# Kernel optimization log

Measured on AMD Instinct MI355X. Metric: run time of the kernel, lower is better.

Reference implementation:

```python
import jax, jax.numpy as jnp
import numpy as np

D_MODEL = 256
SCALE = jnp.sqrt(jnp.float32(D_MODEL))


def setup_inputs() -> dict:
    key = jax.random.key(0)
    kq, kk, kv = jax.random.split(key, 3)
    B, S, D = 4, 4096, D_MODEL
    Q = jax.random.normal(kq, (B, S, D), dtype=jnp.float32)
    K = jax.random.normal(kk, (B, S, D), dtype=jnp.float32)
    V = jax.random.normal(kv, (B, S, D), dtype=jnp.float32)
    return {"Q": Q, "K": K, "V": V}


def reference(Q, K, V):
    # scores: (B, S, S) = Q @ K^T / sqrt(d_model)
    scores = jnp.einsum('bqd,bkd->bqk', Q, K) / SCALE
    attn = jax.nn.softmax(scores, axis=-1)
    # output: (B, S, D)
    return jnp.einsum('bqk,bkd->bqd', attn, V)
```

## Files before the change

kernel.cpp:

```cpp
#include <hip/hip_runtime.h>
#include <hip/hip_bf16.h>
#include <stdint.h>

#define S_LEN 4096
#define D_DIM 256
#define NBATCH 4
#define NKT 64
#define NSUP 32

typedef unsigned short u16;
typedef float  f32x4  __attribute__((ext_vector_type(4)));
typedef __bf16 bf16x8 __attribute__((ext_vector_type(8)));
typedef __bf16 bf16x4 __attribute__((ext_vector_type(4)));
typedef short  s16x8  __attribute__((ext_vector_type(8)));
typedef short  s16x4  __attribute__((ext_vector_type(4)));

__device__ __forceinline__ f32x4 mfma16(bf16x8 a, bf16x8 b, f32x4 c) {
  return __builtin_amdgcn_mfma_f32_16x16x32_bf16(a, b, c, 0, 0, 0);
}

__device__ __forceinline__ s16x4 cvt4(float x, float y, float z, float w) {
  bf16x4 b;
  b[0] = (__bf16)x; b[1] = (__bf16)y; b[2] = (__bf16)z; b[3] = (__bf16)w;
  return __builtin_bit_cast(s16x4, b);
}

__global__ void convert_bf16_kernel(const float* __restrict__ in,
                                    u16* __restrict__ out, int n4) {
  int i = blockIdx.x * blockDim.x + threadIdx.x;
  if (i >= n4) return;
  float4 f = reinterpret_cast<const float4*>(in)[i];
  reinterpret_cast<s16x4*>(out)[i] = cvt4(f.x, f.y, f.z, f.w);
}


__device__ __forceinline__
void compute_tile(const char* KsB, const char* vpA, const char* vpB,
                  const bf16x8 (&qf)[8], f32x4 (&acc)[16],
                  float& m_run, float& l_run, int g, int h)
{
  const f32x4 fz = {0.f, 0.f, 0.f, 0.f};

  f32x4 st[4];
  __builtin_amdgcn_s_setprio(1);
  #pragma unroll
  for (int t = 0; t < 4; ++t) {
    f32x4 a = fz;
    const int row = t * 16 + h;
    const int sw  = (row & 7) << 4;
    #pragma unroll
    for (int dc = 0; dc < 8; ++dc) {
      s16x8 kfrag = *reinterpret_cast<const s16x8*>(KsB + row * 512 + ((dc * 64 + g * 16) ^ sw));
      a = mfma16(__builtin_bit_cast(bf16x8, kfrag), qf[dc], a);
    }
    st[t] = a;
  }
  __builtin_amdgcn_s_setprio(0);

  float sv[16];
  #pragma unroll
  for (int t = 0; t < 4; ++t) {
    sv[t * 4 + 0] = st[t][0]; sv[t * 4 + 1] = st[t][1];
    sv[t * 4 + 2] = st[t][2]; sv[t * 4 + 3] = st[t][3];
  }
  float tmax = sv[0];
  #pragma unroll
  for (int i = 1; i < 16; ++i) tmax = fmaxf(tmax, sv[i]);
  tmax = fmaxf(tmax, __shfl_xor(tmax, 16));
  tmax = fmaxf(tmax, __shfl_xor(tmax, 32));

  if (!__all(tmax <= m_run + 8.0f)) {
    const float mnew  = fmaxf(m_run, tmax);
    const float alpha = __expf(m_run - mnew);
    l_run *= alpha;
    const float af0 = __shfl(alpha, g * 4 + 0);
    const float af1 = __shfl(alpha, g * 4 + 1);
    const float af2 = __shfl(alpha, g * 4 + 2);
    const float af3 = __shfl(alpha, g * 4 + 3);
    #pragma unroll
    for (int dt = 0; dt < 16; ++dt) {
      acc[dt][0] *= af0; acc[dt][1] *= af1; acc[dt][2] *= af2; acc[dt][3] *= af3;
    }
    m_run = mnew;
  }

  float psum = 0.f;
  #pragma unroll
  for (int i = 0; i < 16; ++i) { sv[i] = __expf(sv[i] - m_run); psum += sv[i]; }
  psum += __shfl_xor(psum, 16);
  psum += __shfl_xor(psum, 32);
  l_run += psum;

  bf16x8 pa0, pa1;
  #pragma unroll
  for (int j = 0; j < 8; ++j) { pa0[j] = (__bf16)sv[j]; pa1[j] = (__bf16)sv[8 + j]; }

  __builtin_amdgcn_s_setprio(1);
  #pragma unroll
  for (int dt = 0; dt < 16; ++dt) {
    s16x8 v0 = *reinterpret_cast<const s16x8*>(vpA + dt * 2048);
    s16x8 v1 = *reinterpret_cast<const s16x8*>(vpB + dt * 2048);
    acc[dt] = mfma16(pa0, __builtin_bit_cast(bf16x8, v0), acc[dt]);
    acc[dt] = mfma16(pa1, __builtin_bit_cast(bf16x8, v1), acc[dt]);
  }
  __builtin_amdgcn_s_setprio(0);
}

template<bool USE_WS>
__global__ __launch_bounds__(512, 1)
void attn_fwd_kernel(const float* __restrict__ Qg, const void* __restrict__ Kp,
                     const void* __restrict__ Vp, float* __restrict__ Og)
{
  __shared__ __align__(16) char smem[131072];

  const int wg   = blockIdx.x;
  const int swz  = (wg & 7) * 32 + (wg >> 3);
  const int b    = swz >> 6;
  const int qt   = swz & 63;
  const int tid  = threadIdx.x;
  const int wave = tid >> 6;
  const int lane = tid & 63;
  const int g    = lane >> 4;
  const int h    = lane & 15;
  const int gid  = tid >> 8;
  const int ltid = tid & 255;
  const int wq   = wave & 3;

  const int kb  = ltid & 15;
  const int dcq = ltid >> 4;

  char* KsB = smem + gid * 65536;
  char* VtB = KsB + 32768;

  const int qbase = qt * 64 + wq * 16;

  bf16x8 qf[8];
  {
    const float* qrow = Qg + ((size_t)b * S_LEN + qbase + h) * D_DIM;
    #pragma unroll
    for (int dc = 0; dc < 8; ++dc) {
      float4 f0 = *reinterpret_cast<const float4*>(qrow + dc * 32 + g * 8);
      float4 f1 = *reinterpret_cast<const float4*>(qrow + dc * 32 + g * 8 + 4);
      bf16x8 q;
      q[0] = (__bf16)(f0.x * 0.0625f); q[1] = (__bf16)(f0.y * 0.0625f);
      q[2] = (__bf16)(f0.z * 0.0625f); q[3] = (__bf16)(f0.w * 0.0625f);
      q[4] = (__bf16)(f1.x * 0.0625f); q[5] = (__bf16)(f1.y * 0.0625f);
      q[6] = (__bf16)(f1.z * 0.0625f); q[7] = (__bf16)(f1.w * 0.0625f);
      qf[dc] = q;
    }
  }

  f32x4 acc[16];
  const f32x4 fz = {0.f, 0.f, 0.f, 0.f};
  #pragma unroll
  for (int i = 0; i < 16; ++i) acc[i] = fz;
  float m_run = -1e30f;
  float l_run = 0.f;

  const char* vpA = VtB + h * 128 + ((32 * g)      ^ ((h & 7) << 4));
  const char* vpB = VtB + h * 128 + ((32 * g + 16) ^ ((h & 7) << 4));

  if constexpr (USE_WS) {
    const u16* Kb = (const u16*)Kp + (size_t)b * S_LEN * D_DIM;
    const u16* Vb = (const u16*)Vp + (size_t)b * S_LEN * D_DIM;

    const u16* ksrc = Kb + (size_t)(ltid >> 5) * D_DIM + (ltid & 31) * 8;
    char*      kdst = KsB + (ltid >> 5) * 512 + (((ltid & 31) * 16) ^ ((ltid >> 5) << 4));
    const u16* vsrc = Vb + (size_t)(kb * 4) * D_DIM + dcq * 16;
    const int  Xw   = 32 * (kb & 3) + 8 * (kb >> 2);

    s16x8 kreg[8], vlo[4], vhi[4];

    {
      const size_t nb = (size_t)gid * 64 * D_DIM;
      #pragma unroll
      for (int i = 0; i < 8; ++i)
        kreg[i] = *reinterpret_cast<const s16x8*>(ksrc + nb + (size_t)i * 8 * D_DIM);
      #pragma unroll
      for (int r = 0; r < 4; ++r) {
        const u16* s = vsrc + nb + (size_t)r * D_DIM;
        vlo[r] = *reinterpret_cast<const s16x8*>(s);
        vhi[r] = *reinterpret_cast<const s16x8*>(s + 8);
      }
      #pragma unroll
      for (int i = 0; i < 8; ++i)
        *reinterpret_cast<s16x8*>(kdst + i * 4096) = kreg[i];
      #pragma unroll
      for (int j = 0; j < 8; ++j) {
        s16x4 c0, c1;
        c0[0] = vlo[0][j]; c0[1] = vlo[1][j]; c0[2] = vlo[2][j]; c0[3] = vlo[3][j];
        c1[0] = vhi[0][j]; c1[1] = vhi[1][j]; c1[2] = vhi[2][j]; c1[3] = vhi[3][j];
        const int d0 = dcq * 16 + j;
        const int d1 = d0 + 8;
        *reinterpret_cast<s16x4*>(VtB + d0 * 128 + (Xw ^ ((d0 & 7) << 4))) = c0;
        *reinterpret_cast<s16x4*>(VtB + d1 * 128 + (Xw ^ ((d1 & 7) << 4))) = c1;
      }
    }
    __syncthreads();

    for (int s = 0; s < NSUP - 1; ++s) {
      const size_t nb = (size_t)(2 * (s + 1) + gid) * 64 * D_DIM;
      #pragma unroll
      for (int i = 0; i < 8; ++i)
        kreg[i] = *reinterpret_cast<const s16x8*>(ksrc + nb + (size_t)i * 8 * D_DIM);
      #pragma unroll
      for (int r = 0; r < 4; ++r) {
        const u16* sp = vsrc + nb + (size_t)r * D_DIM;
        vlo[r] = *reinterpret_cast<const s16x8*>(sp);
        vhi[r] = *reinterpret_cast<const s16x8*>(sp + 8);
      }

      compute_tile(KsB, vpA, vpB, qf, acc, m_run, l_run, g, h);

      __syncthreads();
      #pragma unroll
      for (int i = 0; i < 8; ++i)
        *reinterpret_cast<s16x8*>(kdst + i * 4096) = kreg[i];
      #pragma unroll
      for (int j = 0; j < 8; ++j) {
        s16x4 c0, c1;
        c0[0] = vlo[0][j]; c0[1] = vlo[1][j]; c0[2] = vlo[2][j]; c0[3] = vlo[3][j];
        c1[0] = vhi[0][j]; c1[1] = vhi[1][j]; c1[2] = vhi[2][j]; c1[3] = vhi[3][j];
        const int d0 = dcq * 16 + j;
        const int d1 = d0 + 8;
        *reinterpret_cast<s16x4*>(VtB + d0 * 128 + (Xw ^ ((d0 & 7) << 4))) = c0;
        *reinterpret_cast<s16x4*>(VtB + d1 * 128 + (Xw ^ ((d1 & 7) << 4))) = c1;
      }
      __syncthreads();
    }
    compute_tile(KsB, vpA, vpB, qf, acc, m_run, l_run, g, h);

  } else {
    const float* Kf = (const float*)Kp + (size_t)b * S_LEN * D_DIM;
    const float* Vf = (const float*)Vp + (size_t)b * S_LEN * D_DIM;
    for (int s = 0; s < NSUP; ++s) {
      const int kt = 2 * s + gid;
      __syncthreads();
      #pragma unroll
      for (int i = 0; i < 16; ++i) {
        int flat = i * 256 + ltid;
        int kk = flat >> 6;
        int d  = (flat & 63) * 4;
        float4 fk = *reinterpret_cast<const float4*>(Kf + (size_t)(kt * 64 + kk) * D_DIM + d);
        *reinterpret_cast<s16x4*>(KsB + kk * 512 + ((d * 2) ^ ((kk & 7) << 4))) = cvt4(fk.x, fk.y, fk.z, fk.w);
      }
      {
        s16x8 lo[4], hi[4];
        #pragma unroll
        for (int r = 0; r < 4; ++r) {
          const float* src = Vf + (size_t)(kt * 64 + kb * 4 + r) * D_DIM + dcq * 16;
          float4 f0 = *reinterpret_cast<const float4*>(src);
          float4 f1 = *reinterpret_cast<const float4*>(src + 4);
          float4 f2 = *reinterpret_cast<const float4*>(src + 8);
          float4 f3 = *reinterpret_cast<const float4*>(src + 12);
          lo[r] = __builtin_shufflevector(cvt4(f0.x, f0.y, f0.z, f0.w),
                                          cvt4(f1.x, f1.y, f1.z, f1.w), 0, 1, 2, 3, 4, 5, 6, 7);
          hi[r] = __builtin_shufflevector(cvt4(f2.x, f2.y, f2.z, f2.w),
                                          cvt4(f3.x, f3.y, f3.z, f3.w), 0, 1, 2, 3, 4, 5, 6, 7);
        }
        const int Xw = 32 * (kb & 3) + 8 * (kb >> 2);
        #pragma unroll
        for (int j = 0; j < 8; ++j) {
          s16x4 c0, c1;
          c0[0] = lo[0][j]; c0[1] = lo[1][j]; c0[2] = lo[2][j]; c0[3] = lo[3][j];
          c1[0] = hi[0][j]; c1[1] = hi[1][j]; c1[2] = hi[2][j]; c1[3] = hi[3][j];
          const int d0 = dcq * 16 + j;
          const int d1 = d0 + 8;
          *reinterpret_cast<s16x4*>(VtB + d0 * 128 + (Xw ^ ((d0 & 7) << 4))) = c0;
          *reinterpret_cast<s16x4*>(VtB + d1 * 128 + (Xw ^ ((d1 & 7) << 4))) = c1;
        }
      }
      __syncthreads();
      compute_tile(KsB, vpA, vpB, qf, acc, m_run, l_run, g, h);
    }
  }

  __syncthreads();
  float2* mlM = reinterpret_cast<float2*>(smem + 65536);
  if (gid == 1) {
    const int bw = wave - 4;
    char* base = smem + bw * 16384 + lane * 256;
    #pragma unroll
    for (int dt = 0; dt < 16; ++dt) {
      float4 v; v.x = acc[dt][0]; v.y = acc[dt][1]; v.z = acc[dt][2]; v.w = acc[dt][3];
      *reinterpret_cast<float4*>(base + (dt * 16 ^ ((lane & 7) << 4))) = v;
    }
    if (g == 0) { float2 ml; ml.x = m_run; ml.y = l_run; mlM[bw * 16 + h] = ml; }
  }
  __syncthreads();
  if (gid == 0) {
    const float2 ml = mlM[wave * 16 + h];
    const float mB = ml.x, lB = ml.y;
    const float m  = fmaxf(m_run, mB);
    const float sA = __expf(m_run - m);
    const float sB = __expf(mB - m);
    const float l  = l_run * sA + lB * sB;
    float aA[4], aB[4], inv[4];
    #pragma unroll
    for (int r = 0; r < 4; ++r) {
      aA[r]  = __shfl(sA, g * 4 + r);
      aB[r]  = __shfl(sB, g * 4 + r);
      inv[r] = 1.f / __shfl(l, g * 4 + r);
    }
    const char* base = smem + wave * 16384 + lane * 256;
    float* orow0 = Og + ((size_t)b * S_LEN + qbase) * D_DIM;
    #pragma unroll
    for (int dt = 0; dt < 16; ++dt) {
      float4 ab = *reinterpret_cast<const float4*>(base + (dt * 16 ^ ((lane & 7) << 4)));
      orow0[(size_t)(g * 4 + 0) * D_DIM + h + dt * 16] = (acc[dt][0] * aA[0] + ab.x * aB[0]) * inv[0];
      orow0[(size_t)(g * 4 + 1) * D_DIM + h + dt * 16] = (acc[dt][1] * aA[1] + ab.y * aB[1]) * inv[1];
      orow0[(size_t)(g * 4 + 2) * D_DIM + h + dt * 16] = (acc[dt][2] * aA[2] + ab.z * aB[2]) * inv[2];
      orow0[(size_t)(g * 4 + 3) * D_DIM + h + dt * 16] = (acc[dt][3] * aA[3] + ab.w * aB[3]) * inv[3];
    }
  }
}

extern "C" void kernel_launch(void* const* d_in, const int* in_sizes, int n_in,
                              void* d_out, int out_size, void* d_ws, size_t ws_size,
                              hipStream_t stream)
{
  const float* Q = (const float*)d_in[0];
  const float* K = (const float*)d_in[1];
  const float* V = (const float*)d_in[2];
  float* O = (float*)d_out;

  const size_t nelem = (size_t)NBATCH * S_LEN * D_DIM;
  const size_t need  = 2 * nelem * sizeof(u16);

  if (ws_size >= need) {
    u16* Kb = (u16*)d_ws;
    u16* Vb = Kb + nelem;
    int n4 = (int)(nelem / 4);
    convert_bf16_kernel<<<n4 / 256, 256, 0, stream>>>(K, Kb, n4);
    convert_bf16_kernel<<<n4 / 256, 256, 0, stream>>>(V, Vb, n4);
    attn_fwd_kernel<true><<<256, 512, 0, stream>>>(Q, (const void*)Kb, (const void*)Vb, O);
  } else {
    attn_fwd_kernel<false><<<256, 512, 0, stream>>>(Q, (const void*)K, (const void*)V, O);
  }
}
```

Measured before the change: 152.8 us.

## Split KV across four wave groups with 32-row tiles and two query subtiles per wave

Each wave now processes two 16-row query subtiles, so every K and V fragment read from LDS feeds two MFMAs. The KV range is split into four interleaved streams of 32-row tiles instead of two streams of 64-row tiles, and the partial results are combined in a two-stage tree at the end. K tiles are now copied straight from global memory into LDS with global_load_lds instead of passing through registers. The aim is to cut LDS read traffic and register staging, but it doubles accumulator registers and adds merge synchronisation. It also declares launch_bounds(512,2) while using about 130 KB of LDS, which is likely to leave one block per CU anyway.

```diff
diff --git a/kernel.cpp b/kernel.cpp
--- a/kernel.cpp
+++ b/kernel.cpp
@@ -5,7 +5,8 @@
 #define S_LEN 4096
 #define D_DIM 256
 #define NBATCH 4
-#define NKT 64
+#define KVBLK 32
+#define NT 128
 #define NSUP 32
 
 typedef unsigned short u16;
@@ -15,6 +16,9 @@
 typedef short  s16x8  __attribute__((ext_vector_type(8)));
 typedef short  s16x4  __attribute__((ext_vector_type(4)));
 
+#define AS1 __attribute__((address_space(1)))
+#define AS3 __attribute__((address_space(3)))
+
 __device__ __forceinline__ f32x4 mfma16(bf16x8 a, bf16x8 b, f32x4 c) {
   return __builtin_amdgcn_mfma_f32_16x16x32_bf16(a, b, c, 0, 0, 0);
 }
@@ -23,6 +27,11 @@
   bf16x4 b;
   b[0] = (__bf16)x; b[1] = (__bf16)y; b[2] = (__bf16)z; b[3] = (__bf16)w;
   return __builtin_bit_cast(s16x4, b);
+}
+
+__device__ __forceinline__ void gload16(const void* g, void* l) {
+  __builtin_amdgcn_global_load_lds((const AS1 unsigned int*)g,
+                                   (AS3 unsigned int*)l, 16, 0, 0);
 }
 
 __global__ void convert_bf16_kernel(const float* __restrict__ in,
@@ -35,83 +44,86 @@
 
 
 __device__ __forceinline__
-void compute_tile(const char* KsB, const char* vpA, const char* vpB,
-                  const bf16x8 (&qf)[8], f32x4 (&acc)[16],
-                  float& m_run, float& l_run, int g, int h)
+void compute_tile2(const char* KsB, const char* VtB,
+                   const bf16x8 (&qf)[2][8], f32x4 (&acc)[2][16],
+                   float (&m_run)[2], float (&l_run)[2], int g, int h)
 {
   const f32x4 fz = {0.f, 0.f, 0.f, 0.f};
 
-  f32x4 st[4];
+  f32x4 st[2][2];
+  st[0][0] = fz; st[0][1] = fz; st[1][0] = fz; st[1][1] = fz;
   __builtin_amdgcn_s_setprio(1);
   #pragma unroll
-  for (int t = 0; t < 4; ++t) {
-    f32x4 a = fz;
+  for (int t = 0; t < 2; ++t) {
     const int row = t * 16 + h;
     const int sw  = (row & 7) << 4;
     #pragma unroll
     for (int dc = 0; dc < 8; ++dc) {
-      s16x8 kfrag = *reinterpret_cast<const s16x8*>(KsB + row * 512 + ((dc * 64 + g * 16) ^ sw));
-      a = mfma16(__builtin_bit_cast(bf16x8, kfrag), qf[dc], a);
-    }
-    st[t] = a;
+      s16x8 kf = *reinterpret_cast<const s16x8*>(KsB + row * 512 + ((dc * 64 + g * 16) ^ sw));
+      st[0][t] = mfma16(__builtin_bit_cast(bf16x8, kf), qf[0][dc], st[0][t]);
+      st[1][t] = mfma16(__builtin_bit_cast(bf16x8, kf), qf[1][dc], st[1][t]);
+    }
   }
   __builtin_amdgcn_s_setprio(0);
 
-  float sv[16];
+  bf16x8 pa[2];
   #pragma unroll
-  for (int t = 0; t < 4; ++t) {
-    sv[t * 4 + 0] = st[t][0]; sv[t * 4 + 1] = st[t][1];
-    sv[t * 4 + 2] = st[t][2]; sv[t * 4 + 3] = st[t][3];
-  }
-  float tmax = sv[0];
-  #pragma unroll
-  for (int i = 1; i < 16; ++i) tmax = fmaxf(tmax, sv[i]);
-  tmax = fmaxf(tmax, __shfl_xor(tmax, 16));
-  tmax = fmaxf(tmax, __shfl_xor(tmax, 32));
-
-  if (!__all(tmax <= m_run + 8.0f)) {
-    const float mnew  = fmaxf(m_run, tmax);
-    const float alpha = __expf(m_run - mnew);
-    l_run *= alpha;
-    const float af0 = __shfl(alpha, g * 4 + 0);
-    const float af1 = __shfl(alpha, g * 4 + 1);
-    const float af2 = __shfl(alpha, g * 4 + 2);
-    const float af3 = __shfl(alpha, g * 4 + 3);
-    #pragma unroll
-    for (int dt = 0; dt < 16; ++dt) {
-      acc[dt][0] *= af0; acc[dt][1] *= af1; acc[dt][2] *= af2; acc[dt][3] *= af3;
-    }
-    m_run = mnew;
-  }
-
-  float psum = 0.f;
-  #pragma unroll
-  for (int i = 0; i < 16; ++i) { sv[i] = __expf(sv[i] - m_run); psum += sv[i]; }
-  psum += __shfl_xor(psum, 16);
-  psum += __shfl_xor(psum, 32);
-  l_run += psum;
-
-  bf16x8 pa0, pa1;
-  #pragma unroll
-  for (int j = 0; j < 8; ++j) { pa0[j] = (__bf16)sv[j]; pa1[j] = (__bf16)sv[8 + j]; }
+  for (int qs = 0; qs < 2; ++qs) {
+    float sv[8];
+    #pragma unroll
+    for (int t = 0; t < 2; ++t) {
+      sv[t * 4 + 0] = st[qs][t][0]; sv[t * 4 + 1] = st[qs][t][1];
+      sv[t * 4 + 2] = st[qs][t][2]; sv[t * 4 + 3] = st[qs][t][3];
+    }
+    float tmax = sv[0];
+    #pragma unroll
+    for (int i = 1; i < 8; ++i) tmax = fmaxf(tmax, sv[i]);
+    tmax = fmaxf(tmax, __shfl_xor(tmax, 16));
+    tmax = fmaxf(tmax, __shfl_xor(tmax, 32));
+
+    if (!__all(tmax <= m_run[qs] + 8.0f)) {
+      const float mnew  = fmaxf(m_run[qs], tmax);
+      const float alpha = __expf(m_run[qs] - mnew);
+      l_run[qs] *= alpha;
+      float af[4];
+      #pragma unroll
+      for (int r = 0; r < 4; ++r) af[r] = __shfl(alpha, g * 4 + r);
+      #pragma unroll
+      for (int dt = 0; dt < 16; ++dt) {
+        acc[qs][dt][0] *= af[0]; acc[qs][dt][1] *= af[1];
+        acc[qs][dt][2] *= af[2]; acc[qs][dt][3] *= af[3];
+      }
+      m_run[qs] = mnew;
+    }
+
+    float psum = 0.f;
+    #pragma unroll
+    for (int i = 0; i < 8; ++i) { sv[i] = __expf(sv[i] - m_run[qs]); psum += sv[i]; }
+    psum += __shfl_xor(psum, 16);
+    psum += __shfl_xor(psum, 32);
+    l_run[qs] += psum;
+
+    #pragma unroll
+    for (int j = 0; j < 8; ++j) pa[qs][j] = (__bf16)sv[j];
+  }
 
   __builtin_amdgcn_s_setprio(1);
   #pragma unroll
   for (int dt = 0; dt < 16; ++dt) {
-    s16x8 v0 = *reinterpret_cast<const s16x8*>(vpA + dt * 2048);
-    s16x8 v1 = *reinterpret_cast<const s16x8*>(vpB + dt * 2048);
-    acc[dt] = mfma16(pa0, __builtin_bit_cast(bf16x8, v0), acc[dt]);
-    acc[dt] = mfma16(pa1, __builtin_bit_cast(bf16x8, v1), acc[dt]);
+    const int d = dt * 16 + h;
+    s16x8 vf = *reinterpret_cast<const s16x8*>(VtB + d * 64 + ((16 * g) ^ (((dt ^ h) & 3) << 4)));
+    acc[0][dt] = mfma16(pa[0], __builtin_bit_cast(bf16x8, vf), acc[0][dt]);
+    acc[1][dt] = mfma16(pa[1], __builtin_bit_cast(bf16x8, vf), acc[1][dt]);
   }
   __builtin_amdgcn_s_setprio(0);
 }
 
 template<bool USE_WS>
-__global__ __launch_bounds__(512, 1)
+__global__ __launch_bounds__(512, 2)
 void attn_fwd_kernel(const float* __restrict__ Qg, const void* __restrict__ Kp,
                      const void* __restrict__ Vp, float* __restrict__ Og)
 {
-  __shared__ __align__(16) char smem[131072];
+  __shared__ __align__(16) char smem[133120];
 
   const int wg   = blockIdx.x;
   const int swz  = (wg & 7) * 32 + (wg >> 3);
@@ -122,21 +134,24 @@
   const int lane = tid & 63;
   const int g    = lane >> 4;
   const int h    = lane & 15;
-  const int gid  = tid >> 8;
-  const int ltid = tid & 255;
-  const int wq   = wave & 3;
-
-  const int kb  = ltid & 15;
-  const int dcq = ltid >> 4;
-
-  char* KsB = smem + gid * 65536;
-  char* VtB = KsB + 32768;
-
-  const int qbase = qt * 64 + wq * 16;
-
-  bf16x8 qf[8];
-  {
-    const float* qrow = Qg + ((size_t)b * S_LEN + qbase + h) * D_DIM;
+  const int gid  = wave >> 1;
+  const int wq   = wave & 1;
+  const int ltid = tid & 127;
+
+  const int kb  = ltid & 7;
+  const int dcq = ltid >> 3;
+  const int Xw  = 16 * (kb & 3) + 8 * (kb >> 2);
+
+  char* KsB = smem + gid * 32768;
+  char* VtB = KsB + 16384;
+  float2* mlS = reinterpret_cast<float2*>(smem + 131072);
+
+  const int qbase = qt * 64 + wq * 32;
+
+  bf16x8 qf[2][8];
+  #pragma unroll
+  for (int qs = 0; qs < 2; ++qs) {
+    const float* qrow = Qg + ((size_t)b * S_LEN + qbase + qs * 16 + h) * D_DIM;
     #pragma unroll
     for (int dc = 0; dc < 8; ++dc) {
       float4 f0 = *reinterpret_cast<const float4*>(qrow + dc * 32 + g * 8);
@@ -146,45 +161,45 @@
       q[2] = (__bf16)(f0.z * 0.0625f); q[3] = (__bf16)(f0.w * 0.0625f);
       q[4] = (__bf16)(f1.x * 0.0625f); q[5] = (__bf16)(f1.y * 0.0625f);
       q[6] = (__bf16)(f1.z * 0.0625f); q[7] = (__bf16)(f1.w * 0.0625f);
-      qf[dc] = q;
-    }
-  }
-
-  f32x4 acc[16];
+      qf[qs][dc] = q;
+    }
+  }
+
+  f32x4 acc[2][16];
   const f32x4 fz = {0.f, 0.f, 0.f, 0.f};
   #pragma unroll
-  for (int i = 0; i < 16; ++i) acc[i] = fz;
-  float m_run = -1e30f;
-  float l_run = 0.f;
-
-  const char* vpA = VtB + h * 128 + ((32 * g)      ^ ((h & 7) << 4));
-  const char* vpB = VtB + h * 128 + ((32 * g + 16) ^ ((h & 7) << 4));
+  for (int qs = 0; qs < 2; ++qs)
+    #pragma unroll
+    for (int i = 0; i < 16; ++i) acc[qs][i] = fz;
+  float m_run[2] = {-1e30f, -1e30f};
+  float l_run[2] = {0.f, 0.f};
 
   if constexpr (USE_WS) {
     const u16* Kb = (const u16*)Kp + (size_t)b * S_LEN * D_DIM;
     const u16* Vb = (const u16*)Vp + (size_t)b * S_LEN * D_DIM;
 
-    const u16* ksrc = Kb + (size_t)(ltid >> 5) * D_DIM + (ltid & 31) * 8;
-    char*      kdst = KsB + (ltid >> 5) * 512 + (((ltid & 31) * 16) ^ ((ltid >> 5) << 4));
+    const int kb0     = wq * 16 + (lane >> 5);
+    const int colbase = (lane & 31) * 8;
+
     const u16* vsrc = Vb + (size_t)(kb * 4) * D_DIM + dcq * 16;
-    const int  Xw   = 32 * (kb & 3) + 8 * (kb >> 2);
-
-    s16x8 kreg[8], vlo[4], vhi[4];
+
+    s16x8 vlo[4], vhi[4];
 
     {
-      const size_t nb = (size_t)gid * 64 * D_DIM;
-      #pragma unroll
-      for (int i = 0; i < 8; ++i)
-        kreg[i] = *reinterpret_cast<const s16x8*>(ksrc + nb + (size_t)i * 8 * D_DIM);
+      const u16* kt_ptr = Kb + (size_t)gid * KVBLK * D_DIM;
+      #pragma unroll
+      for (int i = 0; i < 8; ++i) {
+        const int k = kb0 + 2 * i;
+        gload16(kt_ptr + k * 256 + (colbase ^ ((k & 7) << 3)),
+                KsB + wq * 8192 + i * 1024);
+      }
+      const size_t nb = (size_t)gid * KVBLK * D_DIM;
       #pragma unroll
       for (int r = 0; r < 4; ++r) {
         const u16* s = vsrc + nb + (size_t)r * D_DIM;
         vlo[r] = *reinterpret_cast<const s16x8*>(s);
         vhi[r] = *reinterpret_cast<const s16x8*>(s + 8);
       }
-      #pragma unroll
-      for (int i = 0; i < 8; ++i)
-        *reinterpret_cast<s16x8*>(kdst + i * 4096) = kreg[i];
       #pragma unroll
       for (int j = 0; j < 8; ++j) {
         s16x4 c0, c1;
@@ -192,17 +207,14 @@
         c1[0] = vhi[0][j]; c1[1] = vhi[1][j]; c1[2] = vhi[2][j]; c1[3] = vhi[3][j];
         const int d0 = dcq * 16 + j;
         const int d1 = d0 + 8;
-        *reinterpret_cast<s16x4*>(VtB + d0 * 128 + (Xw ^ ((d0 & 7) << 4))) = c0;
-        *reinterpret_cast<s16x4*>(VtB + d1 * 128 + (Xw ^ ((d1 & 7) << 4))) = c1;
+        *reinterpret_cast<s16x4*>(VtB + d0 * 64 + (Xw ^ ((((d0 >> 4) ^ d0) & 3) << 4))) = c0;
+        *reinterpret_cast<s16x4*>(VtB + d1 * 64 + (Xw ^ ((((d1 >> 4) ^ d1) & 3) << 4))) = c1;
       }
     }
     __syncthreads();
 
     for (int s = 0; s < NSUP - 1; ++s) {
-      const size_t nb = (size_t)(2 * (s + 1) + gid) * 64 * D_DIM;
-      #pragma unroll
-      for (int i = 0; i < 8; ++i)
-        kreg[i] = *reinterpret_cast<const s16x8*>(ksrc + nb + (size_t)i * 8 * D_DIM);
+      const size_t nb = (size_t)(4 * (s + 1) + gid) * KVBLK * D_DIM;
       #pragma unroll
       for (int r = 0; r < 4; ++r) {
         const u16* sp = vsrc + nb + (size_t)r * D_DIM;
@@ -210,12 +222,18 @@
         vhi[r] = *reinterpret_cast<const s16x8*>(sp + 8);
       }
 
-      compute_tile(KsB, vpA, vpB, qf, acc, m_run, l_run, g, h);
+      compute_tile2(KsB, VtB, qf, acc, m_run, l_run, g, h);
 
       __syncthreads();
-      #pragma unroll
-      for (int i = 0; i < 8; ++i)
-        *reinterpret_cast<s16x8*>(kdst + i * 4096) = kreg[i];
+      {
+        const u16* kt_ptr = Kb + nb;
+        #pragma unroll
+        for (int i = 0; i < 8; ++i) {
+          const int k = kb0 + 2 * i;
+          gload16(kt_ptr + k * 256 + (colbase ^ ((k & 7) << 3)),
+                  KsB + wq * 8192 + i * 1024);
+        }
+      }
       #pragma unroll
       for (int j = 0; j < 8; ++j) {
         s16x4 c0, c1;
@@ -223,32 +241,34 @@
         c1[0] = vhi[0][j]; c1[1] = vhi[1][j]; c1[2] = vhi[2][j]; c1[3] = vhi[3][j];
         const int d0 = dcq * 16 + j;
         const int d1 = d0 + 8;
-        *reinterpret_cast<s16x4*>(VtB + d0 * 128 + (Xw ^ ((d0 & 7) << 4))) = c0;
-        *reinterpret_cast<s16x4*>(VtB + d1 * 128 + (Xw ^ ((d1 & 7) << 4))) = c1;
+        *reinterpret_cast<s16x4*>(VtB + d0 * 64 + (Xw ^ ((((d0 >> 4) ^ d0) & 3) << 4))) = c0;
+        *reinterpret_cast<s16x4*>(VtB + d1 * 64 + (Xw ^ ((((d1 >> 4) ^ d1) & 3) << 4))) = c1;
       }
       __syncthreads();
     }
-    compute_tile(KsB, vpA, vpB, qf, acc, m_run, l_run, g, h);
+    compute_tile2(KsB, VtB, qf, acc, m_run, l_run, g, h);
 
   } else {
     const float* Kf = (const float*)Kp + (size_t)b * S_LEN * D_DIM;
     const float* Vf = (const float*)Vp + (size_t)b * S_LEN * D_DIM;
+    const int rk = ltid >> 2, ck = ltid & 3;
     for (int s = 0; s < NSUP; ++s) {
-      const int kt = 2 * s + gid;
+      const int tile = 4 * s + gid;
       __syncthreads();
       #pragma unroll
-      for (int i = 0; i < 16; ++i) {
-        int flat = i * 256 + ltid;
-        int kk = flat >> 6;
-        int d  = (flat & 63) * 4;
-        float4 fk = *reinterpret_cast<const float4*>(Kf + (size_t)(kt * 64 + kk) * D_DIM + d);
-        *reinterpret_cast<s16x4*>(KsB + kk * 512 + ((d * 2) ^ ((kk & 7) << 4))) = cvt4(fk.x, fk.y, fk.z, fk.w);
+      for (int i = 0; i < 8; ++i) {
+        const float* src = Kf + (size_t)(tile * KVBLK + rk) * D_DIM + ck * 64 + i * 8;
+        float4 f0 = *reinterpret_cast<const float4*>(src);
+        float4 f1 = *reinterpret_cast<const float4*>(src + 4);
+        char* dst = KsB + rk * 512 + ((ck * 128 + i * 16) ^ ((rk & 7) << 4));
+        *reinterpret_cast<s16x4*>(dst)     = cvt4(f0.x, f0.y, f0.z, f0.w);
+        *reinterpret_cast<s16x4*>(dst + 8) = cvt4(f1.x, f1.y, f1.z, f1.w);
       }
       {
         s16x8 lo[4], hi[4];
         #pragma unroll
         for (int r = 0; r < 4; ++r) {
-          const float* src = Vf + (size_t)(kt * 64 + kb * 4 + r) * D_DIM + dcq * 16;
+          const float* src = Vf + (size_t)(tile * KVBLK + kb * 4 + r) * D_DIM + dcq * 16;
           float4 f0 = *reinterpret_cast<const float4*>(src);
           float4 f1 = *reinterpret_cast<const float4*>(src + 4);
           float4 f2 = *reinterpret_cast<const float4*>(src + 8);
@@ -258,7 +278,6 @@
           hi[r] = __builtin_shufflevector(cvt4(f2.x, f2.y, f2.z, f2.w),
                                           cvt4(f3.x, f3.y, f3.z, f3.w), 0, 1, 2, 3, 4, 5, 6, 7);
         }
-        const int Xw = 32 * (kb & 3) + 8 * (kb >> 2);
         #pragma unroll
         for (int j = 0; j < 8; ++j) {
           s16x4 c0, c1;
@@ -266,51 +285,94 @@
           c1[0] = hi[0][j]; c1[1] = hi[1][j]; c1[2] = hi[2][j]; c1[3] = hi[3][j];
           const int d0 = dcq * 16 + j;
           const int d1 = d0 + 8;
-          *reinterpret_cast<s16x4*>(VtB + d0 * 128 + (Xw ^ ((d0 & 7) << 4))) = c0;
-          *reinterpret_cast<s16x4*>(VtB + d1 * 128 + (Xw ^ ((d1 & 7) << 4))) = c1;
+          *reinterpret_cast<s16x4*>(VtB + d0 * 64 + (Xw ^ ((((d0 >> 4) ^ d0) & 3) << 4))) = c0;
+          *reinterpret_cast<s16x4*>(VtB + d1 * 64 + (Xw ^ ((((d1 >> 4) ^ d1) & 3) << 4))) = c1;
         }
       }
       __syncthreads();
-      compute_tile(KsB, vpA, vpB, qf, acc, m_run, l_run, g, h);
+      compute_tile2(KsB, VtB, qf, acc, m_run, l_run, g, h);
     }
   }
 
   __syncthreads();
-  float2* mlM = reinterpret_cast<float2*>(smem + 65536);
+  if (gid >= 2) {
+    char* base = smem + ((gid - 2) * 2 + wq) * 32768 + lane * 512;
+    #pragma unroll
+    for (int qs = 0; qs < 2; ++qs)
+      #pragma unroll
+      for (int dt = 0; dt < 16; ++dt)
+        *reinterpret_cast<f32x4*>(base + (((qs * 16 + dt) * 16) ^ ((lane & 7) << 4))) = acc[qs][dt];
+    if (lane < 16) {
+      float2 a; a.x = m_run[0]; a.y = l_run[0]; mlS[wave * 32 + lane]      = a;
+      float2 c; c.x = m_run[1]; c.y = l_run[1]; mlS[wave * 32 + 16 + lane] = c;
+    }
+  }
+  __syncthreads();
+  if (gid < 2) {
+    const int pw = (gid + 2) * 2 + wq;
+    const char* base = smem + (gid * 2 + wq) * 32768 + lane * 512;
+    #pragma unroll
+    for (int qs = 0; qs < 2; ++qs) {
+      const float2 mlB = mlS[pw * 32 + qs * 16 + h];
+      const float mN = fmaxf(m_run[qs], mlB.x);
+      const float sA = __expf(m_run[qs] - mN);
+      const float sB = __expf(mlB.x - mN);
+      l_run[qs] = l_run[qs] * sA + mlB.y * sB;
+      m_run[qs] = mN;
+      float aA[4], aB[4];
+      #pragma unroll
+      for (int r = 0; r < 4; ++r) { aA[r] = __shfl(sA, g * 4 + r); aB[r] = __shfl(sB, g * 4 + r); }
+      #pragma unroll
+      for (int dt = 0; dt < 16; ++dt) {
+        f32x4 ab = *reinterpret_cast<const f32x4*>(base + (((qs * 16 + dt) * 16) ^ ((lane & 7) << 4)));
+        acc[qs][dt][0] = acc[qs][dt][0] * aA[0] + ab[0] * aB[0];
+        acc[qs][dt][1] = acc[qs][dt][1] * aA[1] + ab[1] * aB[1];
+        acc[qs][dt][2] = acc[qs][dt][2] * aA[2] + ab[2] * aB[2];
+        acc[qs][dt][3] = acc[qs][dt][3] * aA[3] + ab[3] * aB[3];
+      }
+    }
+  }
+  __syncthreads();
   if (gid == 1) {
-    const int bw = wave - 4;
-    char* base = smem + bw * 16384 + lane * 256;
-    #pragma unroll
-    for (int dt = 0; dt < 16; ++dt) {
-      float4 v; v.x = acc[dt][0]; v.y = acc[dt][1]; v.z = acc[dt][2]; v.w = acc[dt][3];
-      *reinterpret_cast<float4*>(base + (dt * 16 ^ ((lane & 7) << 4))) = v;
-    }
-    if (g == 0) { float2 ml; ml.x = m_run; ml.y = l_run; mlM[bw * 16 + h] = ml; }
+    char* base = smem + wq * 32768 + lane * 512;
+    #pragma unroll
+    for (int qs = 0; qs < 2; ++qs)
+      #pragma unroll
+      for (int dt = 0; dt < 16; ++dt)
+        *reinterpret_cast<f32x4*>(base + (((qs * 16 + dt) * 16) ^ ((lane & 7) << 4))) = acc[qs][dt];
+    if (lane < 16) {
+      float2 a; a.x = m_run[0]; a.y = l_run[0]; mlS[wave * 32 + lane]      = a;
+      float2 c; c.x = m_run[1]; c.y = l_run[1]; mlS[wave * 32 + 16 + lane] = c;
+    }
   }
   __syncthreads();
   if (gid == 0) {
-    const float2 ml = mlM[wave * 16 + h];
-    const float mB = ml.x, lB = ml.y;
-    const float m  = fmaxf(m_run, mB);
-    const float sA = __expf(m_run - m);
-    const float sB = __expf(mB - m);
-    const float l  = l_run * sA + lB * sB;
-    float aA[4], aB[4], inv[4];
-    #pragma unroll
-    for (int r = 0; r < 4; ++r) {
-      aA[r]  = __shfl(sA, g * 4 + r);
-      aB[r]  = __shfl(sB, g * 4 + r);
-      inv[r] = 1.f / __shfl(l, g * 4 + r);
-    }
-    const char* base = smem + wave * 16384 + lane * 256;
+    const int pw = 2 + wq;
+    const char* base = smem + wq * 32768 + lane * 512;
     float* orow0 = Og + ((size_t)b * S_LEN + qbase) * D_DIM;
     #pragma unroll
-    for (int dt = 0; dt < 16; ++dt) {
-      float4 ab = *reinterpret_cast<const float4*>(base + (dt * 16 ^ ((lane & 7) << 4)));
-      orow0[(size_t)(g * 4 + 0) * D_DIM + h + dt * 16] = (acc[dt][0] * aA[0] + ab.x * aB[0]) * inv[0];
-      orow0[(size_t)(g * 4 + 1) * D_DIM + h + dt * 16] = (acc[dt][1] * aA[1] + ab.y * aB[1]) * inv[1];
-      orow0[(size_t)(g * 4 + 2) * D_DIM + h + dt * 16] = (acc[dt][2] * aA[2] + ab.z * aB[2]) * inv[2];
-      orow0[(size_t)(g * 4 + 3) * D_DIM + h + dt * 16] = (acc[dt][3] * aA[3] + ab.w * aB[3]) * inv[3];
+    for (int qs = 0; qs < 2; ++qs) {
+      const float2 mlB = mlS[pw * 32 + qs * 16 + h];
+      const float mN = fmaxf(m_run[qs], mlB.x);
+      const float sA = __expf(m_run[qs] - mN);
+      const float sB = __expf(mlB.x - mN);
+      const float lN = l_run[qs] * sA + mlB.y * sB;
+      float aA[4], aB[4], inv[4];
+      #pragma unroll
+      for (int r = 0; r < 4; ++r) {
+        aA[r]  = __shfl(sA, g * 4 + r);
+        aB[r]  = __shfl(sB, g * 4 + r);
+        inv[r] = 1.f / __shfl(lN, g * 4 + r);
+      }
+      #pragma unroll
+      for (int dt = 0; dt < 16; ++dt) {
+        f32x4 ab = *reinterpret_cast<const f32x4*>(base + (((qs * 16 + dt) * 16) ^ ((lane & 7) << 4)));
+        #pragma unroll
+        for (int r = 0; r < 4; ++r) {
+          orow0[(size_t)(qs * 16 + g * 4 + r) * D_DIM + dt * 16 + h] =
+              (acc[qs][dt][r] * aA[r] + ab[r] * aB[r]) * inv[r];
+        }
+      }
     }
   }
 }
```

New measurement: 273.1 us. 78.7% more time.

## Ping-pong compute and tile staging between the two thread groups

Applied to the files above, without the earlier changes.

Replaces register-prefetch double buffering with a schedule where the two 256-thread groups alternate: one group computes on its smem tile while the other stages the next K/V tile into its own buffer. This removes the live prefetch registers and aims to hide global-load latency behind compute. In exchange, only half the waves issue MFMA at any given time, which may serialize the matrix work.

```diff
diff --git a/kernel.cpp b/kernel.cpp
--- a/kernel.cpp
+++ b/kernel.cpp
@@ -104,6 +104,36 @@
     acc[dt] = mfma16(pa1, __builtin_bit_cast(bf16x8, v1), acc[dt]);
   }
   __builtin_amdgcn_s_setprio(0);
+}
+
+__device__ __forceinline__
+void stage_tile(int T, const u16* ksrc, char* kdst,
+                const u16* vsrc, char* VtB, int Xw, int dcq)
+{
+  const size_t nb = (size_t)T * 64 * D_DIM;
+  s16x8 kreg[8], vlo[4], vhi[4];
+  #pragma unroll
+  for (int i = 0; i < 8; ++i)
+    kreg[i] = *reinterpret_cast<const s16x8*>(ksrc + nb + (size_t)i * 8 * D_DIM);
+  #pragma unroll
+  for (int r = 0; r < 4; ++r) {
+    const u16* s = vsrc + nb + (size_t)r * D_DIM;
+    vlo[r] = *reinterpret_cast<const s16x8*>(s);
+    vhi[r] = *reinterpret_cast<const s16x8*>(s + 8);
+  }
+  #pragma unroll
+  for (int i = 0; i < 8; ++i)
+    *reinterpret_cast<s16x8*>(kdst + i * 4096) = kreg[i];
+  #pragma unroll
+  for (int j = 0; j < 8; ++j) {
+    s16x4 c0, c1;
+    c0[0] = vlo[0][j]; c0[1] = vlo[1][j]; c0[2] = vlo[2][j]; c0[3] = vlo[3][j];
+    c1[0] = vhi[0][j]; c1[1] = vhi[1][j]; c1[2] = vhi[2][j]; c1[3] = vhi[3][j];
+    const int d0 = dcq * 16 + j;
+    const int d1 = d0 + 8;
+    *reinterpret_cast<s16x4*>(VtB + d0 * 128 + (Xw ^ ((d0 & 7) << 4))) = c0;
+    *reinterpret_cast<s16x4*>(VtB + d1 * 128 + (Xw ^ ((d1 & 7) << 4))) = c1;
+  }
 }
 
 template<bool USE_WS>
@@ -128,6 +158,7 @@
 
   const int kb  = ltid & 15;
   const int dcq = ltid >> 4;
+  const int Xw  = 32 * (kb & 3) + 8 * (kb >> 2);
 
   char* KsB = smem + gid * 65536;
   char* VtB = KsB + 32768;
@@ -167,68 +198,18 @@
     const u16* ksrc = Kb + (size_t)(ltid >> 5) * D_DIM + (ltid & 31) * 8;
     char*      kdst = KsB + (ltid >> 5) * 512 + (((ltid & 31) * 16) ^ ((ltid >> 5) << 4));
     const u16* vsrc = Vb + (size_t)(kb * 4) * D_DIM + dcq * 16;
-    const int  Xw   = 32 * (kb & 3) + 8 * (kb >> 2);
-
-    s16x8 kreg[8], vlo[4], vhi[4];
-
-    {
-      const size_t nb = (size_t)gid * 64 * D_DIM;
-      #pragma unroll
-      for (int i = 0; i < 8; ++i)
-        kreg[i] = *reinterpret_cast<const s16x8*>(ksrc + nb + (size_t)i * 8 * D_DIM);
-      #pragma unroll
-      for (int r = 0; r < 4; ++r) {
-        const u16* s = vsrc + nb + (size_t)r * D_DIM;
-        vlo[r] = *reinterpret_cast<const s16x8*>(s);
-        vhi[r] = *reinterpret_cast<const s16x8*>(s + 8);
-      }
-      #pragma unroll
-      for (int i = 0; i < 8; ++i)
-        *reinterpret_cast<s16x8*>(kdst + i * 4096) = kreg[i];
-      #pragma unroll
-      for (int j = 0; j < 8; ++j) {
-        s16x4 c0, c1;
-        c0[0] = vlo[0][j]; c0[1] = vlo[1][j]; c0[2] = vlo[2][j]; c0[3] = vlo[3][j];
-        c1[0] = vhi[0][j]; c1[1] = vhi[1][j]; c1[2] = vhi[2][j]; c1[3] = vhi[3][j];
-        const int d0 = dcq * 16 + j;
-        const int d1 = d0 + 8;
-        *reinterpret_cast<s16x4*>(VtB + d0 * 128 + (Xw ^ ((d0 & 7) << 4))) = c0;
-        *reinterpret_cast<s16x4*>(VtB + d1 * 128 + (Xw ^ ((d1 & 7) << 4))) = c1;
-      }
-    }
+
+    if (gid == 0) stage_tile(0, ksrc, kdst, vsrc, VtB, Xw, dcq);
     __syncthreads();
 
-    for (int s = 0; s < NSUP - 1; ++s) {
-      const size_t nb = (size_t)(2 * (s + 1) + gid) * 64 * D_DIM;
-      #pragma unroll
-      for (int i = 0; i < 8; ++i)
-        kreg[i] = *reinterpret_cast<const s16x8*>(ksrc + nb + (size_t)i * 8 * D_DIM);
-      #pragma unroll
-      for (int r = 0; r < 4; ++r) {
-        const u16* sp = vsrc + nb + (size_t)r * D_DIM;
-        vlo[r] = *reinterpret_cast<const s16x8*>(sp);
-        vhi[r] = *reinterpret_cast<const s16x8*>(sp + 8);
-      }
-
-      compute_tile(KsB, vpA, vpB, qf, acc, m_run, l_run, g, h);
-
+    for (int s = 0; s < NSUP; ++s) {
+      if (gid == 0) compute_tile(KsB, vpA, vpB, qf, acc, m_run, l_run, g, h);
+      else          stage_tile(2 * s + 1, ksrc, kdst, vsrc, VtB, Xw, dcq);
       __syncthreads();
-      #pragma unroll
-      for (int i = 0; i < 8; ++i)
-        *reinterpret_cast<s16x8*>(kdst + i * 4096) = kreg[i];
-      #pragma unroll
-      for (int j = 0; j < 8; ++j) {
-        s16x4 c0, c1;
-        c0[0] = vlo[0][j]; c0[1] = vlo[1][j]; c0[2] = vlo[2][j]; c0[3] = vlo[3][j];
-        c1[0] = vhi[0][j]; c1[1] = vhi[1][j]; c1[2] = vhi[2][j]; c1[3] = vhi[3][j];
-        const int d0 = dcq * 16 + j;
-        const int d1 = d0 + 8;
-        *reinterpret_cast<s16x4*>(VtB + d0 * 128 + (Xw ^ ((d0 & 7) << 4))) = c0;
-        *reinterpret_cast<s16x4*>(VtB + d1 * 128 + (Xw ^ ((d1 & 7) << 4))) = c1;
-      }
+      if (gid == 0) { if (s < NSUP - 1) stage_tile(2 * s + 2, ksrc, kdst, vsrc, VtB, Xw, dcq); }
+      else          compute_tile(KsB, vpA, vpB, qf, acc, m_run, l_run, g, h);
       __syncthreads();
     }
-    compute_tile(KsB, vpA, vpB, qf, acc, m_run, l_run, g, h);
 
   } else {
     const float* Kf = (const float*)Kp + (size_t)b * S_LEN * D_DIM;
@@ -258,7 +239,6 @@
           hi[r] = __builtin_shufflevector(cvt4(f2.x, f2.y, f2.z, f2.w),
                                           cvt4(f3.x, f3.y, f3.z, f3.w), 0, 1, 2, 3, 4, 5, 6, 7);
         }
-        const int Xw = 32 * (kb & 3) + 8 * (kb >> 2);
         #pragma unroll
         for (int j = 0; j < 8; ++j) {
           s16x4 c0, c1;
```

Measured after the change: 134.0 us. 1.14x faster.
